# Kernel tuning notes

Hardware: AMD Instinct MI355X
Metric: run time of the kernel (lower is better)

## Reference

```python
import jax, jax.numpy as jnp
import numpy as np

B, GNN_DIM, TR_DIM, F = 16384, 512, 768, 1024


def setup_inputs() -> dict:
    key = jax.random.key(0)
    ks = jax.random.split(key, 16)
    s = 0.02
    return {
        "gnn_features": jax.random.normal(ks[0], (B, GNN_DIM), jnp.float32),
        "transformer_features": jax.random.normal(ks[1], (B, TR_DIM), jnp.float32),
        # gnn_projector / transformer_projector (torch Linear: y = x @ W.T + b)
        "Wg": jax.random.normal(ks[2], (F, GNN_DIM), jnp.float32) * s,
        "bg": jnp.zeros((F,), jnp.float32),
        "Wt": jax.random.normal(ks[3], (F, TR_DIM), jnp.float32) * s,
        "bt": jnp.zeros((F,), jnp.float32),
        # MultiheadAttention value-projection slice of in_proj_weight and out_proj.
        # With seq_len==1 the softmax over a single key is identically 1, so the
        # attention output is exactly out_proj(v_proj(key)); Q/K projections do
        # not affect the output (their gradients are exactly zero).
        "Wv": jax.random.normal(ks[4], (F, F), jnp.float32) * s,
        "bv": jnp.zeros((F,), jnp.float32),
        "Wo": jax.random.normal(ks[5], (F, F), jnp.float32) * s,
        "bo": jnp.zeros((F,), jnp.float32),
        # fusion_layers: Linear(2F -> F), GELU, Dropout(eval: identity), Linear(F -> F)
        "W1": jax.random.normal(ks[6], (F, 2 * F), jnp.float32) * s,
        "b1": jnp.zeros((F,), jnp.float32),
        "W2": jax.random.normal(ks[7], (F, F), jnp.float32) * s,
        "b2": jnp.zeros((F,), jnp.float32),
    }


def reference(gnn_features, transformer_features, Wg, bg, Wt, bt, Wv, bv, Wo, bo, W1, b1, W2, b2):
    # projections to fusion space  [B, F]
    gnn_proj = gnn_features @ Wg.T + bg
    tr_proj = transformer_features @ Wt.T + bt
    # degenerate single-token cross-attention: softmax over 1 key == 1, so
    # attn(q, k, v=k) = out_proj(v_proj(k)) regardless of the query.
    gnn_attended = (tr_proj @ Wv.T + bv) @ Wo.T + bo   # attention(gnn_seq, tr_seq, tr_seq)
    tr_attended = (gnn_proj @ Wv.T + bv) @ Wo.T + bo   # attention(tr_seq, gnn_seq, gnn_seq)
    combined = jnp.concatenate([gnn_attended, tr_attended], axis=-1)  # [B, 2F]
    h = jax.nn.gelu(combined @ W1.T + b1, approximate=False)          # exact GELU (torch default)
    fused = h @ W2.T + b2
    return fused + gnn_proj + tr_proj
```

## Files before the change

kernel.cpp:

```cpp
#include <hip/hip_runtime.h>
#include <cmath>

#define GAS __attribute__((address_space(1)))
#define LAS __attribute__((address_space(3)))

typedef __bf16 bf16x8 __attribute__((ext_vector_type(8)));
typedef float f32x4 __attribute__((ext_vector_type(4)));

__device__ __forceinline__ void gload16(const void* g, void* l) {
    __builtin_amdgcn_global_load_lds((const GAS void*)g, (LAS void*)l, 16, 0, 0);
}

__global__ void k_prep_convert(const float* __restrict__ gnn, const float* __restrict__ tr,
                               const float* __restrict__ Wo, const float* __restrict__ W1,
                               const float* __restrict__ W2, const float* __restrict__ Wg,
                               const float* __restrict__ Wt,
                               __bf16* __restrict__ X, __bf16* __restrict__ Wo_b,
                               __bf16* __restrict__ W1ab, __bf16* __restrict__ Wp) {
    int b = blockIdx.x;
    const float* src; __bf16* dst; int sld, dld, base, c8;
    if (b < 4096)       { src = gnn;       sld = 512;  dst = X + 1024;        dld = 2304; base = 0;     c8 = 64; }
    else if (b < 10240) { src = tr;        sld = 768;  dst = X + 1536;        dld = 2304; base = 4096;  c8 = 96; }
    else if (b < 10752) { src = Wo;        sld = 1024; dst = Wo_b;            dld = 1024; base = 10240; c8 = 128; }
    else if (b < 11264) { src = W1;        sld = 2048; dst = W1ab;            dld = 1024; base = 10752; c8 = 128; }
    else if (b < 11776) { src = W1 + 1024; sld = 2048; dst = W1ab + 1024*1024; dld = 1024; base = 11264; c8 = 128; }
    else if (b < 12288) { src = W2;        sld = 1024; dst = Wp;              dld = 2304; base = 11776; c8 = 128; }
    else if (b < 12544) { src = Wg;        sld = 512;  dst = Wp + 1024;       dld = 2304; base = 12288; c8 = 64; }
    else                { src = Wt;        sld = 768;  dst = Wp + 1536;       dld = 2304; base = 12544; c8 = 96; }
    int idx = (b - base) * 256 + threadIdx.x;
    int r = idx / c8;
    int c = (idx - r * c8) << 3;
    const float4* s = reinterpret_cast<const float4*>(src + (long)r * sld + c);
    float4 x0 = s[0], x1 = s[1];
    bf16x8 v;
    v[0] = (__bf16)x0.x; v[1] = (__bf16)x0.y; v[2] = (__bf16)x0.z; v[3] = (__bf16)x0.w;
    v[4] = (__bf16)x1.x; v[5] = (__bf16)x1.y; v[6] = (__bf16)x1.z; v[7] = (__bf16)x1.w;
    *reinterpret_cast<bf16x8*>(dst + (long)r * dld + c) = v;
}

__global__ void k_prep_transpose(const float* __restrict__ Wv, const float* __restrict__ Wg,
                                 const float* __restrict__ Wt,
                                 __bf16* __restrict__ WvT, __bf16* __restrict__ WgT,
                                 __bf16* __restrict__ WtT) {
    __shared__ float t[32][33];
    int b = blockIdx.x;
    const float* src; __bf16* dst; int R, C, tile;
    if (b < 1024)      { src = Wv; dst = WvT; R = 1024; C = 1024; tile = b; }
    else if (b < 1536) { src = Wg; dst = WgT; R = 1024; C = 512;  tile = b - 1024; }
    else               { src = Wt; dst = WtT; R = 1024; C = 768;  tile = b - 1536; }
    int tx_n = C >> 5;
    int c0 = (tile % tx_n) << 5, r0 = (tile / tx_n) << 5;
    int tx = threadIdx.x, ty = threadIdx.y;
    #pragma unroll
    for (int i = 0; i < 32; i += 8)
        t[ty + i][tx] = src[(long)(r0 + ty + i) * C + c0 + tx];
    __syncthreads();
    #pragma unroll
    for (int i = 0; i < 32; i += 8)
        dst[(long)(c0 + ty + i) * R + r0 + tx] = (__bf16)t[tx][ty + i];
}

__global__ void k_bias_att(const float* __restrict__ Wo, const float* __restrict__ bv,
                           const float* __restrict__ bo, float* __restrict__ b_att) {
    int i = blockIdx.x;
    float s = 0.f;
    for (int k = threadIdx.x; k < 1024; k += 256) s += Wo[i * 1024 + k] * bv[k];
    __shared__ float red[256];
    red[threadIdx.x] = s;
    __syncthreads();
    for (int off = 128; off > 0; off >>= 1) {
        if (threadIdx.x < off) red[threadIdx.x] += red[threadIdx.x + off];
        __syncthreads();
    }
    if (threadIdx.x == 0) b_att[i] = red[0] + bo[i];
}

__global__ void k_bias_z2(const float* __restrict__ W1, const float* __restrict__ b_att,
                          const float* __restrict__ b1,
                          const __bf16* __restrict__ P, const __bf16* __restrict__ Q,
                          const float* __restrict__ bt, const float* __restrict__ bg,
                          const float* __restrict__ b2,
                          float* __restrict__ bz2, float* __restrict__ b_out) {
    int i = blockIdx.x;
    float s = 0.f;
    for (int k = threadIdx.x; k < 1024; k += 256) {
        s += (W1[(long)i * 2048 + k] + W1[(long)i * 2048 + 1024 + k]) * b_att[k];
        s += (float)P[i * 1024 + k] * bt[k];
        s += (float)Q[i * 1024 + k] * bg[k];
    }
    __shared__ float red[256];
    red[threadIdx.x] = s;
    __syncthreads();
    for (int off = 128; off > 0; off >>= 1) {
        if (threadIdx.x < off) red[threadIdx.x] += red[threadIdx.x + off];
        __syncthreads();
    }
    if (threadIdx.x == 0) {
        bz2[i] = red[0] + b1[i];
        b_out[i] = b2[i] + bg[i] + bt[i];
    }
}

template <int BM, int BN, int MODE>
__global__ __launch_bounds__(256, 2) void k_gemm_nt(
    const __bf16* __restrict__ A, int lda,
    const __bf16* __restrict__ B, int ldb,
    void* __restrict__ Cv, int ldc,
    const float* __restrict__ bias,
    int K, int n_tiles) {
    constexpr int BK = 32;
    constexpr int MR = BM / 32, NR = BN / 32;
    __shared__ alignas(16) __bf16 As[2][BM][BK];
    __shared__ alignas(16) __bf16 Bs[2][BN][BK];

    const int tid = threadIdx.x;
    const int lane = tid & 63;
    const int wave = tid >> 6;

    int bid = blockIdx.x;
    const int nwg = gridDim.x;
    if ((nwg & 7) == 0) bid = (bid & 7) * (nwg >> 3) + (bid >> 3);
    const int bn = bid % n_tiles;
    const int bm = bid / n_tiles;
    const int m0 = bm * BM, n0 = bn * BN;

    const int rp_l = tid >> 2;
    const int sp = tid & 3;

    const int wr = (wave >> 1) * (BM / 2);
    const int wc = (wave & 1) * (BN / 2);
    const int fr = lane & 15;
    const int fb = (lane >> 4) << 4;

    f32x4 acc[MR][NR] = {};
    const int nk = K / BK;

    auto stage = [&](int buf, int kt) {
        char* abase = (char*)&As[buf][0][0];
        char* bbase = (char*)&Bs[buf][0][0];
        #pragma unroll
        for (int it = 0; it < BM / 64; ++it) {
            int rp = it * 64 + rp_l;
            int rl = (rp & ~1) | ((rp ^ (rp >> 2)) & 1);
            int sl = sp ^ (rl & 3);
            gload16(A + (long)(m0 + rl) * lda + kt * BK + sl * 8,
                    abase + it * 4096 + tid * 16);
        }
        #pragma unroll
        for (int it = 0; it < BN / 64; ++it) {
            int rp = it * 64 + rp_l;
            int rl = (rp & ~1) | ((rp ^ (rp >> 2)) & 1);
            int sl = sp ^ (rl & 3);
            gload16(B + (long)(n0 + rl) * ldb + kt * BK + sl * 8,
                    bbase + it * 4096 + tid * 16);
        }
    };

    stage(0, 0);
    for (int kt = 0; kt < nk; ++kt) {
        const int buf = kt & 1;
        __syncthreads();
        if (kt + 1 < nk) stage(buf ^ 1, kt + 1);
        const char* abase = (const char*)&As[buf][0][0];
        const char* bbase = (const char*)&Bs[buf][0][0];
        bf16x8 af[MR], bfr[NR];
        #pragma unroll
        for (int m = 0; m < MR; ++m) {
            int r = wr + m * 16 + fr;
            af[m] = *(const bf16x8*)(abase + (((r << 6) + fb) ^ ((r & 7) << 4)));
        }
        #pragma unroll
        for (int n = 0; n < NR; ++n) {
            int r = wc + n * 16 + fr;
            bfr[n] = *(const bf16x8*)(bbase + (((r << 6) + fb) ^ ((r & 7) << 4)));
        }
        #pragma unroll
        for (int m = 0; m < MR; ++m)
            #pragma unroll
            for (int n = 0; n < NR; ++n)
                acc[m][n] = __builtin_amdgcn_mfma_f32_16x16x32_bf16(af[m], bfr[n], acc[m][n], 0, 0, 0);
    }

    const int r0 = (lane >> 4) << 2;
    #pragma unroll
    for (int n = 0; n < NR; ++n) {
        const int gc = n0 + wc + n * 16 + fr;
        const float bval = (MODE != 0 && bias) ? bias[gc] : 0.0f;
        #pragma unroll
        for (int m = 0; m < MR; ++m) {
            const long rbase = (long)(m0 + wr + m * 16 + r0);
            #pragma unroll
            for (int r = 0; r < 4; ++r) {
                float v = acc[m][n][r] + bval;
                const long row = rbase + r;
                if (MODE == 0) {
                    ((__bf16*)Cv)[row * ldc + gc] = (__bf16)v;
                } else if (MODE == 1) {
                    v = 0.5f * v * (1.0f + erff(v * 0.70710678118f));
                    ((__bf16*)Cv)[row * ldc + gc] = (__bf16)v;
                } else {
                    ((float*)Cv)[row * ldc + gc] = v;
                }
            }
        }
    }
}

extern "C" void kernel_launch(void* const* d_in, const int* in_sizes, int n_in,
                              void* d_out, int out_size, void* d_ws, size_t ws_size,
                              hipStream_t stream) {
    constexpr int Bsz = 16384, F = 1024, GD = 512, TD = 768;
    constexpr int XLD = F + GD + TD;

    const float* gnn = (const float*)d_in[0];
    const float* tr  = (const float*)d_in[1];
    const float* Wg  = (const float*)d_in[2];
    const float* bg  = (const float*)d_in[3];
    const float* Wt  = (const float*)d_in[4];
    const float* bt  = (const float*)d_in[5];
    const float* Wv  = (const float*)d_in[6];
    const float* bv  = (const float*)d_in[7];
    const float* Wo  = (const float*)d_in[8];
    const float* bo  = (const float*)d_in[9];
    const float* W1  = (const float*)d_in[10];
    const float* b1  = (const float*)d_in[11];
    const float* W2  = (const float*)d_in[12];
    const float* b2  = (const float*)d_in[13];
    float* out = (float*)d_out;

    char* w = (char*)d_ws;
    auto alloc = [&](size_t bytes) {
        char* p = w;
        w += (bytes + 255) & ~(size_t)255;
        return p;
    };
    __bf16* X    = (__bf16*)alloc((size_t)Bsz * XLD * 2);
    __bf16* M1   = (__bf16*)alloc((size_t)F * (GD + TD) * 2);
    __bf16* Wp   = (__bf16*)alloc((size_t)F * XLD * 2);
    __bf16* WvT  = (__bf16*)alloc((size_t)F * F * 2);
    __bf16* WgT  = (__bf16*)alloc((size_t)GD * F * 2);
    __bf16* WtT  = (__bf16*)alloc((size_t)TD * F * 2);
    __bf16* Wo_b = (__bf16*)alloc((size_t)F * F * 2);
    __bf16* W1ab = (__bf16*)alloc((size_t)2 * F * F * 2);
    __bf16* AT   = (__bf16*)alloc((size_t)F * F * 2);
    __bf16* PQ   = (__bf16*)alloc((size_t)2 * F * F * 2);
    float* b_att = (float*)alloc(F * 4);
    float* bz2   = (float*)alloc(F * 4);
    float* b_out = (float*)alloc(F * 4);
    if ((size_t)(w - (char*)d_ws) > ws_size) return;

    dim3 b256(256);
    __bf16* P = PQ;
    __bf16* Q = PQ + (size_t)F * F;

    k_prep_convert<<<dim3(12928), b256, 0, stream>>>(gnn, tr, Wo, W1, W2, Wg, Wt,
                                                     X, Wo_b, W1ab, Wp);
    k_prep_transpose<<<dim3(2304), dim3(32, 8), 0, stream>>>(Wv, Wg, Wt, WvT, WgT, WtT);

    k_bias_att<<<dim3(F), b256, 0, stream>>>(Wo, bv, bo, b_att);

    k_gemm_nt<64, 64, 0><<<dim3((F / 64) * (F / 64)), b256, 0, stream>>>(
        WvT, F, Wo_b, F, AT, F, nullptr, F, F / 64);
    k_gemm_nt<64, 64, 0><<<dim3((2 * F / 64) * (F / 64)), b256, 0, stream>>>(
        W1ab, F, AT, F, PQ, F, nullptr, F, F / 64);
    k_gemm_nt<64, 64, 0><<<dim3((F / 64) * (GD / 64)), b256, 0, stream>>>(
        Q, F, WgT, F, M1, GD + TD, nullptr, F, GD / 64);
    k_gemm_nt<64, 64, 0><<<dim3((F / 64) * (TD / 64)), b256, 0, stream>>>(
        P, F, WtT, F, M1 + GD, GD + TD, nullptr, F, TD / 64);

    k_bias_z2<<<dim3(F), b256, 0, stream>>>(W1, b_att, b1, P, Q, bt, bg, b2, bz2, b_out);

    k_gemm_nt<128, 128, 1><<<dim3((Bsz / 128) * (F / 128)), b256, 0, stream>>>(
        X + F, XLD, M1, GD + TD, X, XLD, bz2, GD + TD, F / 128);

    k_gemm_nt<128, 128, 2><<<dim3((Bsz / 128) * (F / 128)), b256, 0, stream>>>(
        X, XLD, Wp, XLD, out, F, b_out, XLD, F / 128);
}
```

Baseline: 246.8 us.

## Add 256x256 eight-wave GEMM with interleaved LDS prefetch for the big GEMMs

The two large batch GEMMs (the GELU layer and the output layer) now use a new kernel with 256x256 tiles, 512 threads (8 waves), a K-step of 64 split into two halves, and double-buffered direct-to-LDS loads interleaved across eight compute phases. Explicit vmcnt waits, barriers and setprio bracket the MFMA bursts. The aim is more reuse per byte loaded and better overlap of global loads with MFMA work than the earlier 128x128 tiles gave. The cost is a much larger LDS footprint and register pressure, only 256 workgroups, and reliance on K being a multiple of 128.

Result: faster. 225.6 us (-8.6%).

```diff
diff --git a/kernel.cpp b/kernel.cpp
--- a/kernel.cpp
+++ b/kernel.cpp
@@ -101,12 +101,11 @@
     }
 }
 
-template <int BM, int BN, int MODE>
+template <int BM, int BN>
 __global__ __launch_bounds__(256, 2) void k_gemm_nt(
     const __bf16* __restrict__ A, int lda,
     const __bf16* __restrict__ B, int ldb,
-    void* __restrict__ Cv, int ldc,
-    const float* __restrict__ bias,
+    __bf16* __restrict__ C, int ldc,
     int K, int n_tiles) {
     constexpr int BK = 32;
     constexpr int MR = BM / 32, NR = BN / 32;
@@ -116,7 +115,6 @@
     const int tid = threadIdx.x;
     const int lane = tid & 63;
     const int wave = tid >> 6;
-
     int bid = blockIdx.x;
     const int nwg = gridDim.x;
     if ((nwg & 7) == 0) bid = (bid & 7) * (nwg >> 3) + (bid >> 3);
@@ -185,17 +183,133 @@
     #pragma unroll
     for (int n = 0; n < NR; ++n) {
         const int gc = n0 + wc + n * 16 + fr;
-        const float bval = (MODE != 0 && bias) ? bias[gc] : 0.0f;
         #pragma unroll
         for (int m = 0; m < MR; ++m) {
             const long rbase = (long)(m0 + wr + m * 16 + r0);
             #pragma unroll
+            for (int r = 0; r < 4; ++r)
+                C[(rbase + r) * ldc + gc] = (__bf16)acc[m][n][r];
+        }
+    }
+}
+
+template <int MODE>
+__global__ __launch_bounds__(512, 2) void k_gemm8(
+    const __bf16* __restrict__ A, int lda,
+    const __bf16* __restrict__ B, int ldb,
+    void* __restrict__ Cv, int ldc,
+    const float* __restrict__ bias,
+    int K, int n_tiles) {
+    __shared__ __bf16 As[2][2][256][32];
+    __shared__ __bf16 Bs[2][2][256][32];
+
+    const int tid = threadIdx.x;
+    const int lane = tid & 63;
+    const int wave = tid >> 6;
+    const int wm = wave >> 2;
+    const int wn = wave & 3;
+
+    int bid = blockIdx.x;
+    const int nwg = gridDim.x;
+    if ((nwg & 7) == 0) bid = (bid & 7) * (nwg >> 3) + (bid >> 3);
+    const int bn = bid % n_tiles;
+    const int bm = bid / n_tiles;
+    const int m0 = bm * 256, n0 = bn * 256;
+
+    const int rp0 = tid >> 2;
+    const int rl0 = (rp0 & ~1) | ((rp0 ^ (rp0 >> 2)) & 1);
+    const int slo = (tid & 3) ^ (rl0 & 3);
+    const __bf16* Ag = A + (long)(m0 + rl0) * lda + slo * 8;
+    const __bf16* Bg = B + (long)(n0 + rl0) * ldb + slo * 8;
+    const long lda128 = (long)128 * lda;
+    const long ldb128 = (long)128 * ldb;
+    const int tid16 = tid * 16;
+
+    const int fr = lane & 15;
+    const int gb = (lane >> 4) << 4;
+
+    f32x4 acc[8][4] = {};
+    bf16x8 bfr[4];
+
+    const int nk = K >> 6;
+    const int NI = nk >> 1;
+
+#define STAGE_A(PAR, KT, KH) { \
+        char* l_ = (char*)&As[PAR][KH][0][0] + tid16; \
+        const __bf16* g_ = Ag + (long)(KT) * 64 + (KH) * 32; \
+        gload16(g_, l_); \
+        gload16(g_ + lda128, l_ + 8192); }
+#define STAGE_B(PAR, KT, KH) { \
+        char* l_ = (char*)&Bs[PAR][KH][0][0] + tid16; \
+        const __bf16* g_ = Bg + (long)(KT) * 64 + (KH) * 32; \
+        gload16(g_, l_); \
+        gload16(g_ + ldb128, l_ + 8192); }
+#define VMC4 asm volatile("s_waitcnt vmcnt(4)" ::: "memory")
+#define VMC0 asm volatile("s_waitcnt vmcnt(0)" ::: "memory")
+#define PHASE(PAR, KS, MH, STAGES, WAITS) { \
+        bf16x8 af[4]; \
+        if ((MH) == 0) { \
+            const char* b_ = (const char*)&Bs[PAR][KS][0][0]; \
+            _Pragma("unroll") \
+            for (int n_ = 0; n_ < 4; ++n_) { \
+                int r_ = wn * 64 + n_ * 16 + fr; \
+                bfr[n_] = *(const bf16x8*)(b_ + (((r_ << 6) + gb) ^ ((r_ & 7) << 4))); } } \
+        { const char* a_ = (const char*)&As[PAR][KS][0][0]; \
+          _Pragma("unroll") \
+          for (int m_ = 0; m_ < 4; ++m_) { \
+              int r_ = wm * 128 + (MH) * 64 + m_ * 16 + fr; \
+              af[m_] = *(const bf16x8*)(a_ + (((r_ << 6) + gb) ^ ((r_ & 7) << 4))); } } \
+        STAGES; \
+        WAITS; \
+        __builtin_amdgcn_s_barrier(); \
+        __builtin_amdgcn_s_setprio(1); \
+        _Pragma("unroll") \
+        for (int m_ = 0; m_ < 4; ++m_) { \
+            _Pragma("unroll") \
+            for (int n_ = 0; n_ < 4; ++n_) \
+                acc[(MH) * 4 + m_][n_] = __builtin_amdgcn_mfma_f32_16x16x32_bf16( \
+                    af[m_], bfr[n_], acc[(MH) * 4 + m_][n_], 0, 0, 0); } \
+        __builtin_amdgcn_s_setprio(0); \
+        __builtin_amdgcn_s_barrier(); }
+
+    STAGE_B(0, 0, 0); STAGE_A(0, 0, 0); STAGE_B(0, 0, 1); STAGE_A(0, 0, 1);
+    STAGE_B(1, 1, 0); STAGE_A(1, 1, 0); STAGE_B(1, 1, 1);
+    VMC4;
+    __builtin_amdgcn_s_barrier();
+
+    for (int I = 0; I < NI; ++I) {
+        const int t = 2 * I;
+        const bool nl = (I < NI - 1);
+        PHASE(0, 0, 0, { STAGE_A(1, t + 1, 1); }, {});
+        PHASE(0, 0, 1, { if (nl) STAGE_B(0, t + 2, 0); }, {});
+        PHASE(0, 1, 0, { if (nl) STAGE_A(0, t + 2, 0); }, {});
+        PHASE(0, 1, 1, { if (nl) STAGE_B(0, t + 2, 1); },
+              { if (nl) { VMC4; } else { VMC0; } });
+        PHASE(1, 0, 0, { if (nl) STAGE_A(0, t + 2, 1); }, {});
+        PHASE(1, 0, 1, { if (nl) STAGE_B(1, t + 3, 0); }, {});
+        PHASE(1, 1, 0, { if (nl) STAGE_A(1, t + 3, 0); }, {});
+        PHASE(1, 1, 1, { if (nl) STAGE_B(1, t + 3, 1); },
+              { if (nl) { VMC4; } });
+    }
+#undef PHASE
+#undef STAGE_A
+#undef STAGE_B
+#undef VMC4
+#undef VMC0
+
+    const int r0q = (lane >> 4) << 2;
+    #pragma unroll
+    for (int n = 0; n < 4; ++n) {
+        const int gc = n0 + wn * 64 + n * 16 + fr;
+        const float bval = bias ? bias[gc] : 0.0f;
+        #pragma unroll
+        for (int mq = 0; mq < 8; ++mq) {
+            const long rbase = (long)(m0 + wm * 128 + mq * 16 + r0q);
+            #pragma unroll
             for (int r = 0; r < 4; ++r) {
-                float v = acc[m][n][r] + bval;
+                float v = acc[mq][n][r] + bval;
                 const long row = rbase + r;
-                if (MODE == 0) {
-                    ((__bf16*)Cv)[row * ldc + gc] = (__bf16)v;
-                } else if (MODE == 1) {
+                if (MODE == 1) {
                     v = 0.5f * v * (1.0f + erff(v * 0.70710678118f));
                     ((__bf16*)Cv)[row * ldc + gc] = (__bf16)v;
                 } else {
@@ -256,23 +370,22 @@
     k_prep_convert<<<dim3(12928), b256, 0, stream>>>(gnn, tr, Wo, W1, W2, Wg, Wt,
                                                      X, Wo_b, W1ab, Wp);
     k_prep_transpose<<<dim3(2304), dim3(32, 8), 0, stream>>>(Wv, Wg, Wt, WvT, WgT, WtT);
-
     k_bias_att<<<dim3(F), b256, 0, stream>>>(Wo, bv, bo, b_att);
 
-    k_gemm_nt<64, 64, 0><<<dim3((F / 64) * (F / 64)), b256, 0, stream>>>(
-        WvT, F, Wo_b, F, AT, F, nullptr, F, F / 64);
-    k_gemm_nt<64, 64, 0><<<dim3((2 * F / 64) * (F / 64)), b256, 0, stream>>>(
-        W1ab, F, AT, F, PQ, F, nullptr, F, F / 64);
-    k_gemm_nt<64, 64, 0><<<dim3((F / 64) * (GD / 64)), b256, 0, stream>>>(
-        Q, F, WgT, F, M1, GD + TD, nullptr, F, GD / 64);
-    k_gemm_nt<64, 64, 0><<<dim3((F / 64) * (TD / 64)), b256, 0, stream>>>(
-        P, F, WtT, F, M1 + GD, GD + TD, nullptr, F, TD / 64);
+    k_gemm_nt<64, 64><<<dim3((F / 64) * (F / 64)), b256, 0, stream>>>(
+        WvT, F, Wo_b, F, AT, F, F, F / 64);
+    k_gemm_nt<64, 64><<<dim3((2 * F / 64) * (F / 64)), b256, 0, stream>>>(
+        W1ab, F, AT, F, PQ, F, F, F / 64);
+    k_gemm_nt<64, 64><<<dim3((F / 64) * (GD / 64)), b256, 0, stream>>>(
+        Q, F, WgT, F, M1, GD + TD, F, GD / 64);
+    k_gemm_nt<64, 64><<<dim3((F / 64) * (TD / 64)), b256, 0, stream>>>(
+        P, F, WtT, F, M1 + GD, GD + TD, F, TD / 64);
 
     k_bias_z2<<<dim3(F), b256, 0, stream>>>(W1, b_att, b1, P, Q, bt, bg, b2, bz2, b_out);
 
-    k_gemm_nt<128, 128, 1><<<dim3((Bsz / 128) * (F / 128)), b256, 0, stream>>>(
-        X + F, XLD, M1, GD + TD, X, XLD, bz2, GD + TD, F / 128);
-
-    k_gemm_nt<128, 128, 2><<<dim3((Bsz / 128) * (F / 128)), b256, 0, stream>>>(
-        X, XLD, Wp, XLD, out, F, b_out, XLD, F / 128);
-}
+    k_gemm8<1><<<dim3((Bsz / 256) * (F / 256)), dim3(512), 0, stream>>>(
+        X + F, XLD, M1, GD + TD, X, XLD, bz2, GD + TD, F / 256);
+
+    k_gemm8<2><<<dim3((Bsz / 256) * (F / 256)), dim3(512), 0, stream>>>(
+        X, XLD, Wp, XLD, out, F, b_out, XLD, F / 256);
+}
```

## Rewrite large GEMMs with fragment-ordered LDS, staged vector epilogue, tanh GELU

Applied to the files above, without the earlier changes.

The two large batch GEMMs move to a new 128x128 kernel body. Global-to-LDS staging is arranged so each lane's MFMA fragment is one contiguous 16-byte LDS read, which removes the XOR swizzle address maths. The epilogue goes through per-wave LDS scratch so stores are coalesced vectors (f32x4 for the output, bf16x8 for the GELU activations) instead of scalar element stores. Other changes: MFMA priority bumps via setprio, launch bounds raised to 4 blocks per CU, and a tanh-based fast GELU replacing exact erf GELU. The tanh GELU trades accuracy against the exact reference for a cheaper epilogue.

Measured after the change: 314.6 us. +27.5%, slower.

```diff
diff --git a/kernel.cpp b/kernel.cpp
--- a/kernel.cpp
+++ b/kernel.cpp
@@ -101,12 +101,11 @@
     }
 }
 
-template <int BM, int BN, int MODE>
+template <int BM, int BN>
 __global__ __launch_bounds__(256, 2) void k_gemm_nt(
     const __bf16* __restrict__ A, int lda,
     const __bf16* __restrict__ B, int ldb,
-    void* __restrict__ Cv, int ldc,
-    const float* __restrict__ bias,
+    __bf16* __restrict__ C, int ldc,
     int K, int n_tiles) {
     constexpr int BK = 32;
     constexpr int MR = BM / 32, NR = BN / 32;
@@ -116,7 +115,6 @@
     const int tid = threadIdx.x;
     const int lane = tid & 63;
     const int wave = tid >> 6;
-
     int bid = blockIdx.x;
     const int nwg = gridDim.x;
     if ((nwg & 7) == 0) bid = (bid & 7) * (nwg >> 3) + (bid >> 3);
@@ -185,25 +183,140 @@
     #pragma unroll
     for (int n = 0; n < NR; ++n) {
         const int gc = n0 + wc + n * 16 + fr;
-        const float bval = (MODE != 0 && bias) ? bias[gc] : 0.0f;
         #pragma unroll
         for (int m = 0; m < MR; ++m) {
             const long rbase = (long)(m0 + wr + m * 16 + r0);
             #pragma unroll
+            for (int r = 0; r < 4; ++r)
+                C[(rbase + r) * ldc + gc] = (__bf16)acc[m][n][r];
+        }
+    }
+}
+
+template <int MODE>
+__device__ __forceinline__ void gemm128_body(
+    const __bf16* __restrict__ A, int lda,
+    const __bf16* __restrict__ B, int ldb,
+    void* __restrict__ Cv, int ldc,
+    const float* __restrict__ bias,
+    int K, int n_tiles) {
+    __shared__ char lds[32768];
+
+    const int tid = threadIdx.x;
+    const int lane = tid & 63;
+    const int wave = tid >> 6;
+    const int wm = wave >> 1;
+    const int wn = wave & 1;
+
+    int bid = blockIdx.x;
+    const int nwg = gridDim.x;
+    if ((nwg & 7) == 0) bid = (bid & 7) * (nwg >> 3) + (bid >> 3);
+    const int bn = bid % n_tiles;
+    const int bm = bid / n_tiles;
+    const int m0 = bm * 128, n0 = bn * 128;
+
+    const int rowS = ((tid >> 6) << 4) + (tid & 15);
+    const int colS = ((tid >> 4) & 3) << 3;
+    const __bf16* Ag = A + (long)(m0 + rowS) * lda + colS;
+    const __bf16* Bg = B + (long)(n0 + rowS) * ldb + colS;
+    const long lda64 = (long)64 * lda;
+    const long ldb64 = (long)64 * ldb;
+    const int tid16 = tid * 16;
+    const int l16 = lane * 16;
+    const int fr = lane & 15;
+
+    f32x4 acc[4][4] = {};
+    const int nk = K >> 5;
+
+    auto stage = [&](int buf, int kt) {
+        const long ko = (long)kt * 32;
+        gload16(Ag + ko,         lds + buf * 8192 + tid16);
+        gload16(Ag + ko + lda64, lds + buf * 8192 + 4096 + tid16);
+        gload16(Bg + ko,         lds + 16384 + buf * 8192 + tid16);
+        gload16(Bg + ko + ldb64, lds + 16384 + buf * 8192 + 4096 + tid16);
+    };
+
+    stage(0, 0);
+    for (int kt = 0; kt < nk; ++kt) {
+        const int buf = kt & 1;
+        __syncthreads();
+        if (kt + 1 < nk) stage(buf ^ 1, kt + 1);
+        const char* a_ = lds + buf * 8192 + (wm * 4) * 1024;
+        const char* b_ = lds + 16384 + buf * 8192 + (wn * 4) * 1024;
+        bf16x8 af[4], bfr[4];
+        #pragma unroll
+        for (int m = 0; m < 4; ++m) af[m] = *(const bf16x8*)(a_ + m * 1024 + l16);
+        #pragma unroll
+        for (int n = 0; n < 4; ++n) bfr[n] = *(const bf16x8*)(b_ + n * 1024 + l16);
+        __builtin_amdgcn_s_setprio(1);
+        #pragma unroll
+        for (int m = 0; m < 4; ++m)
+            #pragma unroll
+            for (int n = 0; n < 4; ++n)
+                acc[m][n] = __builtin_amdgcn_mfma_f32_16x16x32_bf16(af[m], bfr[n], acc[m][n], 0, 0, 0);
+        __builtin_amdgcn_s_setprio(0);
+    }
+    __syncthreads();
+
+    char* scr = lds + wave * 4352;
+    float bval[4];
+    #pragma unroll
+    for (int n_ = 0; n_ < 4; ++n_)
+        bval[n_] = bias ? bias[n0 + wn * 64 + n_ * 16 + fr] : 0.0f;
+    const int r0q = (lane >> 4) << 2;
+
+    #pragma unroll
+    for (int mq = 0; mq < 4; ++mq) {
+        #pragma unroll
+        for (int n_ = 0; n_ < 4; ++n_) {
+            #pragma unroll
             for (int r = 0; r < 4; ++r) {
-                float v = acc[m][n][r] + bval;
-                const long row = rbase + r;
-                if (MODE == 0) {
-                    ((__bf16*)Cv)[row * ldc + gc] = (__bf16)v;
-                } else if (MODE == 1) {
-                    v = 0.5f * v * (1.0f + erff(v * 0.70710678118f));
-                    ((__bf16*)Cv)[row * ldc + gc] = (__bf16)v;
-                } else {
-                    ((float*)Cv)[row * ldc + gc] = v;
+                float v = acc[mq][n_][r] + bval[n_];
+                if (MODE == 1) {
+                    float u = v * (0.7978845608f + 0.0356774081f * v * v);
+                    float e = __expf(-2.0f * fabsf(u));
+                    float th = (1.0f - e) / (1.0f + e);
+                    th = copysignf(th, u);
+                    v = 0.5f * v * (1.0f + th);
                 }
+                *(float*)(scr + (r0q + r) * 272 + (n_ * 16 + fr) * 4) = v;
             }
         }
-    }
+        __builtin_amdgcn_s_waitcnt(0);
+        if (MODE == 2) {
+            #pragma unroll
+            for (int rep = 0; rep < 4; ++rep) {
+                int row = rep * 4 + (lane >> 4);
+                f32x4 val = *(const f32x4*)(scr + row * 272 + (lane & 15) * 16);
+                long grow = (long)(m0 + wm * 64 + mq * 16 + row);
+                *(f32x4*)&((float*)Cv)[grow * ldc + n0 + wn * 64 + (lane & 15) * 4] = val;
+            }
+        } else {
+            #pragma unroll
+            for (int rep = 0; rep < 2; ++rep) {
+                int row = rep * 8 + (lane >> 3);
+                f32x4 v0 = *(const f32x4*)(scr + row * 272 + (lane & 7) * 32);
+                f32x4 v1 = *(const f32x4*)(scr + row * 272 + (lane & 7) * 32 + 16);
+                bf16x8 o;
+                o[0] = (__bf16)v0[0]; o[1] = (__bf16)v0[1]; o[2] = (__bf16)v0[2]; o[3] = (__bf16)v0[3];
+                o[4] = (__bf16)v1[0]; o[5] = (__bf16)v1[1]; o[6] = (__bf16)v1[2]; o[7] = (__bf16)v1[3];
+                long grow = (long)(m0 + wm * 64 + mq * 16 + row);
+                *(bf16x8*)&((__bf16*)Cv)[grow * ldc + n0 + wn * 64 + (lane & 7) * 8] = o;
+            }
+        }
+        __builtin_amdgcn_s_waitcnt(0);
+    }
+}
+
+__global__ __launch_bounds__(256, 4) void k_g128_gelu(
+    const __bf16* __restrict__ A, int lda, const __bf16* __restrict__ B, int ldb,
+    void* __restrict__ Cv, int ldc, const float* __restrict__ bias, int K, int n_tiles) {
+    gemm128_body<1>(A, lda, B, ldb, Cv, ldc, bias, K, n_tiles);
+}
+__global__ __launch_bounds__(256, 4) void k_g128_out(
+    const __bf16* __restrict__ A, int lda, const __bf16* __restrict__ B, int ldb,
+    void* __restrict__ Cv, int ldc, const float* __restrict__ bias, int K, int n_tiles) {
+    gemm128_body<2>(A, lda, B, ldb, Cv, ldc, bias, K, n_tiles);
 }
 
 extern "C" void kernel_launch(void* const* d_in, const int* in_sizes, int n_in,
@@ -256,23 +369,22 @@
     k_prep_convert<<<dim3(12928), b256, 0, stream>>>(gnn, tr, Wo, W1, W2, Wg, Wt,
                                                      X, Wo_b, W1ab, Wp);
     k_prep_transpose<<<dim3(2304), dim3(32, 8), 0, stream>>>(Wv, Wg, Wt, WvT, WgT, WtT);
-
     k_bias_att<<<dim3(F), b256, 0, stream>>>(Wo, bv, bo, b_att);
 
-    k_gemm_nt<64, 64, 0><<<dim3((F / 64) * (F / 64)), b256, 0, stream>>>(
-        WvT, F, Wo_b, F, AT, F, nullptr, F, F / 64);
-    k_gemm_nt<64, 64, 0><<<dim3((2 * F / 64) * (F / 64)), b256, 0, stream>>>(
-        W1ab, F, AT, F, PQ, F, nullptr, F, F / 64);
-    k_gemm_nt<64, 64, 0><<<dim3((F / 64) * (GD / 64)), b256, 0, stream>>>(
-        Q, F, WgT, F, M1, GD + TD, nullptr, F, GD / 64);
-    k_gemm_nt<64, 64, 0><<<dim3((F / 64) * (TD / 64)), b256, 0, stream>>>(
-        P, F, WtT, F, M1 + GD, GD + TD, nullptr, F, TD / 64);
+    k_gemm_nt<64, 64><<<dim3((F / 64) * (F / 64)), b256, 0, stream>>>(
+        WvT, F, Wo_b, F, AT, F, F, F / 64);
+    k_gemm_nt<64, 64><<<dim3((2 * F / 64) * (F / 64)), b256, 0, stream>>>(
+        W1ab, F, AT, F, PQ, F, F, F / 64);
+    k_gemm_nt<64, 64><<<dim3((F / 64) * (GD / 64)), b256, 0, stream>>>(
+        Q, F, WgT, F, M1, GD + TD, F, GD / 64);
+    k_gemm_nt<64, 64><<<dim3((F / 64) * (TD / 64)), b256, 0, stream>>>(
+        P, F, WtT, F, M1 + GD, GD + TD, F, TD / 64);
 
     k_bias_z2<<<dim3(F), b256, 0, stream>>>(W1, b_att, b1, P, Q, bt, bg, b2, bz2, b_out);
 
-    k_gemm_nt<128, 128, 1><<<dim3((Bsz / 128) * (F / 128)), b256, 0, stream>>>(
+    k_g128_gelu<<<dim3((Bsz / 128) * (F / 128)), b256, 0, stream>>>(
         X + F, XLD, M1, GD + TD, X, XLD, bz2, GD + TD, F / 128);
 
-    k_gemm_nt<128, 128, 2><<<dim3((Bsz / 128) * (F / 128)), b256, 0, stream>>>(
+    k_g128_out<<<dim3((Bsz / 128) * (F / 128)), b256, 0, stream>>>(
         X, XLD, Wp, XLD, out, F, b_out, XLD, F / 128);
 }
```
